# Optimization experiments

Hardware: AMD Instinct MI355X
Metric: run time of the kernel (lower is better)

Reference implementation:

```python
import jax, jax.numpy as jnp
import numpy as np

N, E = 10000, 320000
D, H, C = 256, 8, 32   # dim, heads, head_dim (dim//num_head)
DE, DF = 64, 1024      # edge_dim, dim_ff


def setup_inputs() -> dict:
    key = jax.random.key(0)
    ks = jax.random.split(key, 32)
    s = 0.05
    n = lambda k, shp: jax.random.normal(k, shp, jnp.float32) * s
    inp = {
        "nf": jax.random.normal(ks[0], (N, D), jnp.float32),
        "ei": jax.random.randint(ks[1], (2, E), 0, N),
        "ew": jax.random.normal(ks[2], (E, DE), jnp.float32),
        # GATConv 1
        "lin1": n(ks[3], (D, H * C)), "le1": n(ks[4], (DE, H * C)),
        "asrc1": n(ks[5], (H, C)), "adst1": n(ks[6], (H, C)), "aedge1": n(ks[7], (H, C)),
        "b1": jnp.zeros((H * C,), jnp.float32),
        # GATConv 2
        "lin2": n(ks[8], (D, H * C)), "le2": n(ks[9], (DE, H * C)),
        "asrc2": n(ks[10], (H, C)), "adst2": n(ks[11], (H, C)), "aedge2": n(ks[12], (H, C)),
        "b2": jnp.zeros((H * C,), jnp.float32),
        # LayerNorms
        "g1": jnp.ones((D,), jnp.float32), "be1": jnp.zeros((D,), jnp.float32),
        "g2": jnp.ones((D,), jnp.float32), "be2": jnp.zeros((D,), jnp.float32),
        "g3": jnp.ones((D,), jnp.float32), "be3": jnp.zeros((D,), jnp.float32),
        # FFN
        "w1": n(ks[13], (D, DF)), "fb1": jnp.zeros((DF,), jnp.float32),
        "w2": n(ks[14], (DF, D)), "fb2": jnp.zeros((D,), jnp.float32),
    }
    return inp


def _ln(x, g, b, eps=1e-6):
    # annotated-transformer LayerNorm: unbiased std, eps added to std
    mu = x.mean(-1, keepdims=True)
    sd = jnp.std(x, axis=-1, ddof=1, keepdims=True)
    return g * (x - mu) / (sd + eps) + b


def _gat(x, src, dst, ea, W, We, a_s, a_d, a_e, bias):
    # PyG GATConv with edge_dim, add_self_loops=True, fill_value='mean', concat=True
    ones = jnp.ones((src.shape[0], 1), x.dtype)
    cnt = jax.ops.segment_sum(ones, dst, num_segments=N)
    loop_attr = jax.ops.segment_sum(ea, dst, num_segments=N) / jnp.maximum(cnt, 1.0)
    idx = jnp.arange(N)
    srcf = jnp.concatenate([src, idx])
    dstf = jnp.concatenate([dst, idx])
    eaf = jnp.concatenate([ea, loop_attr], axis=0)          # [E+N, DE]
    xs = (x @ W).reshape(N, H, C)                            # [N,H,C]
    ef = (eaf @ We).reshape(-1, H, C)                        # [E+N,H,C]
    a_src = (xs * a_s).sum(-1)                               # [N,H]
    a_dst = (xs * a_d).sum(-1)                               # [N,H]
    alpha = a_src[srcf] + a_dst[dstf] + (ef * a_e).sum(-1)   # [E+N,H]
    alpha = jax.nn.leaky_relu(alpha, 0.2)
    m = jax.ops.segment_max(alpha, dstf, num_segments=N)     # segment softmax
    ex = jnp.exp(alpha - m[dstf])
    den = jax.ops.segment_sum(ex, dstf, num_segments=N)
    w = ex / (den[dstf] + 1e-16)                             # [E+N,H]
    out = jax.ops.segment_sum(w[:, :, None] * xs[srcf], dstf, num_segments=N)
    return out.reshape(N, H * C) + bias


def reference(nf, ei, ew, lin1, le1, asrc1, adst1, aedge1, b1,
              lin2, le2, asrc2, adst2, aedge2, b2,
              g1, be1, g2, be2, g3, be3, w1, fb1, w2, fb2):
    src, dst = ei[0], ei[1]
    h = _gat(nf, src, dst, ew, lin1, le1, asrc1, adst1, aedge1, b1)
    nf = nf + jax.nn.leaky_relu(_ln(h, g1, be1), 0.01)
    h = _gat(nf, src, dst, ew, lin2, le2, asrc2, adst2, aedge2, b2)
    nf = nf + jax.nn.leaky_relu(_ln(h, g2, be2), 0.01)
    h = jax.nn.relu(nf @ w1 + fb1) @ w2 + fb2
    nf = nf + jax.nn.leaky_relu(_ln(h, g3, be3), 0.01)
    return nf
```

## Files before the change

### kernel.cpp

```cpp
#include <hip/hip_runtime.h>
#include <hip/hip_bf16.h>
#include <math.h>

#define D 256
#define H 8
#define C 32
#define DE 64
#define DF 1024

static inline size_t align_up(size_t x, size_t a) { return (x + a - 1) / a * a; }

typedef __attribute__((ext_vector_type(8))) short short8;
typedef __attribute__((ext_vector_type(4))) float f32x4;

__device__ inline unsigned short f2b(float x) {
    __hip_bfloat16 h = __float2bfloat16(x);
    return *reinterpret_cast<unsigned short*>(&h);
}
__device__ inline float b2f(unsigned short u) {
    return __uint_as_float(((unsigned int)u) << 16);
}

__global__ void deg_kernel(const int* __restrict__ dst, int* __restrict__ deg, int E) {
    int e = blockIdx.x * 256 + threadIdx.x;
    if (e < E) atomicAdd(&deg[dst[e]], 1);
}

__global__ void partial_sum_kernel(const int* __restrict__ deg, int* __restrict__ part, int n) {
    int i = blockIdx.x * 256 + threadIdx.x;
    int v = (i < n) ? deg[i] : 0;
    for (int o = 1; o < 64; o <<= 1) v += __shfl_xor(v, o);
    __shared__ int w4[4];
    if ((threadIdx.x & 63) == 0) w4[threadIdx.x >> 6] = v;
    __syncthreads();
    if (threadIdx.x == 0) part[blockIdx.x] = w4[0] + w4[1] + w4[2] + w4[3];
}

__global__ void scan_part_kernel(int* __restrict__ part, int nb) {
    __shared__ int buf[256];
    int t = threadIdx.x;
    buf[t] = (t < nb) ? part[t] : 0;
    __syncthreads();
    for (int s = 1; s < 256; s <<= 1) {
        int v = (t >= s) ? buf[t - s] : 0;
        __syncthreads();
        buf[t] += v;
        __syncthreads();
    }
    int excl = (t == 0) ? 0 : buf[t - 1];
    if (t < nb) part[t] = excl;
}

__global__ void scan_final_kernel(const int* __restrict__ deg, const int* __restrict__ part,
                                  int* __restrict__ off, int* __restrict__ cursor, int n) {
    int b = blockIdx.x, t = threadIdx.x, i = b * 256 + t;
    __shared__ int buf[256];
    int v = (i < n) ? deg[i] : 0;
    buf[t] = v;
    __syncthreads();
    for (int s = 1; s < 256; s <<= 1) {
        int x = (t >= s) ? buf[t - s] : 0;
        __syncthreads();
        buf[t] += x;
        __syncthreads();
    }
    int excl = part[b] + buf[t] - v;
    if (i < n) { off[i] = excl; cursor[i] = excl; }
    if (i == n - 1) off[n] = excl + v;
}

__global__ void fill_kernel(const int* __restrict__ src, const int* __restrict__ dst,
                            int* __restrict__ cursor, int* __restrict__ eid,
                            int* __restrict__ src_csr, int E) {
    int e = blockIdx.x * 256 + threadIdx.x;
    if (e < E) {
        int p = atomicAdd(&cursor[dst[e]], 1);
        eid[p] = e;
        src_csr[p] = src[e];
    }
}

__global__ void prep_kernel(const float* __restrict__ lin1, const float* __restrict__ lin2,
                            const float* __restrict__ w1, const float* __restrict__ w2,
                            const float* __restrict__ le1, const float* __restrict__ ae1,
                            const float* __restrict__ le2, const float* __restrict__ ae2,
                            const float* __restrict__ nf0,
                            unsigned short* __restrict__ lin1T, unsigned short* __restrict__ lin2T,
                            unsigned short* __restrict__ w1T, unsigned short* __restrict__ w2T,
                            unsigned short* __restrict__ MeT, unsigned short* __restrict__ Abf,
                            size_t n_valid, size_t n_total) {
    int b = blockIdx.x;
    if (b > 640) {
        size_t i = ((size_t)(b - 641) * 256 + threadIdx.x) * 8;
        if (i >= n_total) return;
        ushort4 o0, o1;
        if (i < n_valid) {
            float4 a = *(const float4*)&nf0[i];
            float4 bb = *(const float4*)&nf0[i + 4];
            o0.x = f2b(a.x); o0.y = f2b(a.y); o0.z = f2b(a.z); o0.w = f2b(a.w);
            o1.x = f2b(bb.x); o1.y = f2b(bb.y); o1.z = f2b(bb.z); o1.w = f2b(bb.w);
        } else {
            o0.x = o0.y = o0.z = o0.w = 0;
            o1 = o0;
        }
        *(ushort4*)&Abf[i] = o0;
        *(ushort4*)&Abf[i + 4] = o1;
        return;
    }
    if (b == 640) {
        for (int t = threadIdx.x; t < 512; t += 256) {
            int d = t >> 3, h = t & 7;
            float s1 = 0.f, s2 = 0.f;
            for (int c = 0; c < C; ++c) {
                s1 += le1[d * (H * C) + h * C + c] * ae1[h * C + c];
                s2 += le2[d * (H * C) + h * C + c] * ae2[h * C + c];
            }
            MeT[h * 64 + d] = f2b(s1);
            MeT[(8 + h) * 64 + d] = f2b(s2);
        }
        return;
    }
    __shared__ float tile[32][33];
    const float* in; unsigned short* outp; int K, N, tt;
    if (b < 64)       { in = lin1; outp = lin1T; K = D;  N = D;  tt = b; }
    else if (b < 128) { in = lin2; outp = lin2T; K = D;  N = D;  tt = b - 64; }
    else if (b < 384) { in = w1;   outp = w1T;   K = D;  N = DF; tt = b - 128; }
    else              { in = w2;   outp = w2T;   K = DF; N = D;  tt = b - 384; }
    int ntn = N >> 5;
    int bn = (tt % ntn) * 32, bk = (tt / ntn) * 32;
    int tx = threadIdx.x & 31, ty = threadIdx.x >> 5;
    for (int i = ty; i < 32; i += 8)
        tile[i][tx] = in[(size_t)(bk + i) * N + bn + tx];
    __syncthreads();
    for (int i = ty; i < 32; i += 8)
        outp[(size_t)(bn + i) * K + bk + tx] = f2b(tile[tx][i]);
}

template<int BM>
__global__ __launch_bounds__(256) void mfma_gemm_kernel(
    const unsigned short* __restrict__ A, const unsigned short* __restrict__ BT,
    const float* __restrict__ bias, float* __restrict__ Cf, unsigned short* __restrict__ Cb,
    int M, int Nc, int K, int relu,
    const float* __restrict__ a_s, const float* __restrict__ a_d,
    float* __restrict__ asrcO, float* __restrict__ adstO) {
    constexpr int NR = (BM == 128) ? 4 : 2;
    constexpr int AI = BM / 32;
    __shared__ unsigned short As[BM * 64];
    __shared__ unsigned short Bs[128 * 64];
    int t = threadIdx.x;
    int lane = t & 63, w = t >> 6;
    int gm0 = blockIdx.x * BM, gn0 = blockIdx.y * 128;
    f32x4 acc[4][NR] = {};
    int srow = lane >> 3, scol = (lane & 7) * 8;
    int wm = (BM == 128) ? (w >> 1) * 64 : 0;
    int wn = (BM == 128) ? (w & 1) * 64 : w * 32;
    int fr = lane & 15, fk = (lane >> 4) * 8;

    for (int k0 = 0; k0 < K; k0 += 64) {
        __syncthreads();
#pragma unroll
        for (int i = 0; i < AI; ++i) {
            int rb = w * (8 * AI) + i * 8;
            const unsigned short* ga = A + (size_t)(gm0 + rb + srow) * K + k0 + scol;
            __builtin_amdgcn_global_load_lds(
                (const __attribute__((address_space(1))) unsigned int*)ga,
                (__attribute__((address_space(3))) unsigned int*)&As[rb * 64], 16, 0, 0);
        }
#pragma unroll
        for (int i = 0; i < 4; ++i) {
            int rb = w * 32 + i * 8;
            const unsigned short* gb = BT + (size_t)(gn0 + rb + srow) * K + k0 + scol;
            __builtin_amdgcn_global_load_lds(
                (const __attribute__((address_space(1))) unsigned int*)gb,
                (__attribute__((address_space(3))) unsigned int*)&Bs[rb * 64], 16, 0, 0);
        }
        __syncthreads();
#pragma unroll
        for (int kk = 0; kk < 64; kk += 32) {
            short8 a[4], b[NR];
#pragma unroll
            for (int m = 0; m < 4; ++m)
                a[m] = *(const short8*)&As[(wm + m * 16 + fr) * 64 + kk + fk];
#pragma unroll
            for (int n = 0; n < NR; ++n)
                b[n] = *(const short8*)&Bs[(wn + n * 16 + fr) * 64 + kk + fk];
#pragma unroll
            for (int m = 0; m < 4; ++m)
#pragma unroll
                for (int n = 0; n < NR; ++n)
                    acc[m][n] = __builtin_amdgcn_mfma_f32_16x16x32_bf16(a[m], b[n], acc[m][n], 0, 0, 0);
        }
    }
    int fcol = lane & 15, frow4 = (lane >> 4) * 4;
#pragma unroll
    for (int m = 0; m < 4; ++m) {
#pragma unroll
        for (int i = 0; i < 4; ++i) {
            int gr = gm0 + wm + m * 16 + frow4 + i;
            if (gr >= M) continue;
#pragma unroll
            for (int n = 0; n < NR; ++n) {
                int gc = gn0 + wn + n * 16 + fcol;
                float v = acc[m][n][i];
                if (bias) v += bias[gc];
                if (relu) v = fmaxf(v, 0.f);
                if (Cb) Cb[(size_t)gr * Nc + gc] = f2b(v);
                else    Cf[(size_t)gr * Nc + gc] = v;
            }
        }
    }
    if (BM == 64 && a_s) {
        int head = (gn0 >> 5) + w;
        float as0 = a_s[head * 32 + fcol], as1 = a_s[head * 32 + 16 + fcol];
        float ad0 = a_d[head * 32 + fcol], ad1 = a_d[head * 32 + 16 + fcol];
#pragma unroll
        for (int m = 0; m < 4; ++m) {
#pragma unroll
            for (int i = 0; i < 4; ++i) {
                float vs = acc[m][0][i] * as0 + acc[m][1][i] * as1;
                float vd = acc[m][0][i] * ad0 + acc[m][1][i] * ad1;
#pragma unroll
                for (int o = 1; o < 16; o <<= 1) {
                    vs += __shfl_xor(vs, o);
                    vd += __shfl_xor(vd, o);
                }
                int r = gm0 + m * 16 + frow4 + i;
                if (fcol == 0 && r < M) {
                    asrcO[r * 8 + head] = vs;
                    adstO[r * 8 + head] = vd;
                }
            }
        }
    }
}

__global__ __launch_bounds__(256) void ffn2_ln_kernel(
    const unsigned short* __restrict__ A, const unsigned short* __restrict__ BT,
    const float* __restrict__ bias, const float* __restrict__ nf_in,
    const float* __restrict__ gamma, const float* __restrict__ beta,
    float* __restrict__ out, int M) {
    __shared__ unsigned short As[64 * 64];
    __shared__ unsigned short Bs[256 * 64];
    __shared__ float redS1[4][64], redS2[4][64];
    __shared__ float muS[64], invS[64];
    int t = threadIdx.x, lane = t & 63, w = t >> 6;
    int gm0 = blockIdx.x * 64;
    f32x4 acc[4][4] = {};
    int srow = lane >> 3, scol = (lane & 7) * 8;
    int wn = w * 64;
    int fr = lane & 15, fk = (lane >> 4) * 8;
    for (int k0 = 0; k0 < DF; k0 += 64) {
        __syncthreads();
#pragma unroll
        for (int i = 0; i < 2; ++i) {
            int rb = w * 16 + i * 8;
            const unsigned short* ga = A + (size_t)(gm0 + rb + srow) * DF + k0 + scol;
            __builtin_amdgcn_global_load_lds(
                (const __attribute__((address_space(1))) unsigned int*)ga,
                (__attribute__((address_space(3))) unsigned int*)&As[rb * 64], 16, 0, 0);
        }
#pragma unroll
        for (int i = 0; i < 8; ++i) {
            int rb = w * 64 + i * 8;
            const unsigned short* gb = BT + (size_t)(rb + srow) * DF + k0 + scol;
            __builtin_amdgcn_global_load_lds(
                (const __attribute__((address_space(1))) unsigned int*)gb,
                (__attribute__((address_space(3))) unsigned int*)&Bs[rb * 64], 16, 0, 0);
        }
        __syncthreads();
#pragma unroll
        for (int kk = 0; kk < 64; kk += 32) {
            short8 a[4], b[4];
#pragma unroll
            for (int m = 0; m < 4; ++m)
                a[m] = *(const short8*)&As[(m * 16 + fr) * 64 + kk + fk];
#pragma unroll
            for (int n = 0; n < 4; ++n)
                b[n] = *(const short8*)&Bs[(wn + n * 16 + fr) * 64 + kk + fk];
#pragma unroll
            for (int m = 0; m < 4; ++m)
#pragma unroll
                for (int n = 0; n < 4; ++n)
                    acc[m][n] = __builtin_amdgcn_mfma_f32_16x16x32_bf16(a[m], b[n], acc[m][n], 0, 0, 0);
        }
    }
    int fcol = lane & 15, frow4 = (lane >> 4) * 4;
#pragma unroll
    for (int m = 0; m < 4; ++m) {
#pragma unroll
        for (int i = 0; i < 4; ++i) {
            float vs1 = 0.f, vs2 = 0.f;
#pragma unroll
            for (int n = 0; n < 4; ++n) {
                float vv = acc[m][n][i] + bias[wn + n * 16 + fcol];
                acc[m][n][i] = vv;
                vs1 += vv; vs2 += vv * vv;
            }
#pragma unroll
            for (int o = 1; o < 16; o <<= 1) {
                vs1 += __shfl_xor(vs1, o);
                vs2 += __shfl_xor(vs2, o);
            }
            if (fcol == 0) {
                redS1[w][m * 16 + frow4 + i] = vs1;
                redS2[w][m * 16 + frow4 + i] = vs2;
            }
        }
    }
    __syncthreads();
    if (t < 64) {
        float s1 = redS1[0][t] + redS1[1][t] + redS1[2][t] + redS1[3][t];
        float s2 = redS2[0][t] + redS2[1][t] + redS2[2][t] + redS2[3][t];
        float mu = s1 / 256.f;
        float var = fmaxf((s2 - 256.f * mu * mu) / 255.f, 0.f);
        muS[t] = mu;
        invS[t] = 1.f / (sqrtf(var) + 1e-6f);
    }
    __syncthreads();
#pragma unroll
    for (int m = 0; m < 4; ++m) {
#pragma unroll
        for (int i = 0; i < 4; ++i) {
            int r = m * 16 + frow4 + i;
            int gr = gm0 + r;
            if (gr >= M) continue;
            float mu = muS[r], inv = invS[r];
#pragma unroll
            for (int n = 0; n < 4; ++n) {
                int gc = wn + n * 16 + fcol;
                float y = gamma[gc] * (acc[m][n][i] - mu) * inv + beta[gc];
                y = y > 0.f ? y : 0.01f * y;
                out[(size_t)gr * D + gc] = nf_in[(size_t)gr * D + gc] + y;
            }
        }
    }
}

__global__ __launch_bounds__(256) void ealpha_mfma_kernel(const float* __restrict__ ew,
                                                          const unsigned short* __restrict__ MeT,
                                                          float* __restrict__ eAe, int E) {
    int t = threadIdx.x;
    int lane = t & 63, w = t >> 6;
    int e0 = blockIdx.x * 64 + w * 16;
    int r = lane & 15, g = lane >> 4;
    int er = e0 + r; if (er > E - 1) er = E - 1;
    const float* rowp = ew + (size_t)er * DE;
    float4 x0 = *(const float4*)&rowp[g * 8];
    float4 x1 = *(const float4*)&rowp[g * 8 + 4];
    float4 y0 = *(const float4*)&rowp[32 + g * 8];
    float4 y1 = *(const float4*)&rowp[32 + g * 8 + 4];
    short8 a0, a1;
    a0[0] = (short)f2b(x0.x); a0[1] = (short)f2b(x0.y); a0[2] = (short)f2b(x0.z); a0[3] = (short)f2b(x0.w);
    a0[4] = (short)f2b(x1.x); a0[5] = (short)f2b(x1.y); a0[6] = (short)f2b(x1.z); a0[7] = (short)f2b(x1.w);
    a1[0] = (short)f2b(y0.x); a1[1] = (short)f2b(y0.y); a1[2] = (short)f2b(y0.z); a1[3] = (short)f2b(y0.w);
    a1[4] = (short)f2b(y1.x); a1[5] = (short)f2b(y1.y); a1[6] = (short)f2b(y1.z); a1[7] = (short)f2b(y1.w);
    short8 b0 = *(const short8*)&MeT[r * 64 + g * 8];
    short8 b1 = *(const short8*)&MeT[r * 64 + 32 + g * 8];
    f32x4 acc = {};
    acc = __builtin_amdgcn_mfma_f32_16x16x32_bf16(a0, b0, acc, 0, 0, 0);
    acc = __builtin_amdgcn_mfma_f32_16x16x32_bf16(a1, b1, acc, 0, 0, 0);
#pragma unroll
    for (int i = 0; i < 4; ++i) {
        int ee = e0 + g * 4 + i;
        if (ee < E) eAe[(size_t)ee * 16 + r] = acc[i];
    }
}

__global__ void permute_ea_kernel(const float* __restrict__ eAe, const int* __restrict__ eid,
                                  float* __restrict__ eA1c, float* __restrict__ eA2c, int E) {
    int p = blockIdx.x * 256 + threadIdx.x;
    if (p >= E) return;
    int e = eid[p];
    const float4* src = (const float4*)&eAe[(size_t)e * 16];
    float4 v0 = src[0], v1 = src[1], v2 = src[2], v3 = src[3];
    float4* d1 = (float4*)&eA1c[(size_t)p * 8];
    float4* d2 = (float4*)&eA2c[(size_t)p * 8];
    d1[0] = v0; d1[1] = v1;
    d2[0] = v2; d2[1] = v3;
}

__global__ __launch_bounds__(256) void gat_node_kernel(
    const int* __restrict__ off, const int* __restrict__ src_csr,
    const float* __restrict__ eAc,
    const float* __restrict__ asrc, const float* __restrict__ adst,
    const unsigned short* __restrict__ xsb, const float* __restrict__ nf_in,
    const float* __restrict__ bias, const float* __restrict__ gamma,
    const float* __restrict__ beta, float* __restrict__ nf_out,
    unsigned short* __restrict__ nf_out_b, int N) {
    int lane = threadIdx.x & 63;
    int n = blockIdx.x * 4 + (threadIdx.x >> 6);
    if (n >= N) return;
    int e0 = off[n], e1 = off[n + 1], deg = e1 - e0;
    int h = lane & 7;
    int hw = lane >> 3;

    float adstn = adst[n * 8 + h];
    float asn = asrc[n * 8 + h];

    float acc0 = 0.f, acc1 = 0.f, acc2 = 0.f, acc3 = 0.f;
    float den0 = 0.f, easum = 0.f;
    int nb8 = (deg + 7) >> 3;

    bool act = hw < deg;
    int sp = e0 + hw;
    int s_cur = act ? src_csr[sp] : n;
    float ea_cur = act ? eAc[(size_t)sp * 8 + h] : 0.f;
    float as_cur = act ? asrc[s_cur * 8 + h] : 0.f;

    for (int it = 0; it < nb8; ++it) {
        int base = it * 8;
        bool actn = (base + 8 + hw) < deg;
        int spn = e0 + base + 8 + hw;
        int s_nx = actn ? src_csr[spn] : n;
        float ea_nx = actn ? eAc[(size_t)spn * 8 + h] : 0.f;
        float as_nx = actn ? asrc[s_nx * 8 + h] : 0.f;

        float al = as_cur + adstn + ea_cur;
        al = al > 0.f ? al : 0.2f * al;
        float ex = act ? expf(al) : 0.f;
        den0 += ex;
        easum += ea_cur;

        int lim = deg - base; if (lim > 8) lim = 8;
        if (lim == 8) {
#pragma unroll
            for (int kk = 0; kk < 8; ++kk) {
                int sl = kk * 8 + hw;
                float exk = __shfl(ex, sl);
                int sk = __shfl(s_cur, sl);
                ushort4 u = *(const ushort4*)&xsb[(size_t)sk * D + lane * 4];
                acc0 = fmaf(exk, b2f(u.x), acc0);
                acc1 = fmaf(exk, b2f(u.y), acc1);
                acc2 = fmaf(exk, b2f(u.z), acc2);
                acc3 = fmaf(exk, b2f(u.w), acc3);
            }
        } else {
            for (int kk = 0; kk < lim; ++kk) {
                int sl = kk * 8 + hw;
                float exk = __shfl(ex, sl);
                int sk = __shfl(s_cur, sl);
                ushort4 u = *(const ushort4*)&xsb[(size_t)sk * D + lane * 4];
                acc0 = fmaf(exk, b2f(u.x), acc0);
                acc1 = fmaf(exk, b2f(u.y), acc1);
                acc2 = fmaf(exk, b2f(u.z), acc2);
                acc3 = fmaf(exk, b2f(u.w), acc3);
            }
        }
        s_cur = s_nx; ea_cur = ea_nx; as_cur = as_nx; act = actn;
    }
    den0  += __shfl_xor(den0, 8);
    den0  += __shfl_xor(den0, 16);
    den0  += __shfl_xor(den0, 32);
    easum += __shfl_xor(easum, 8);
    easum += __shfl_xor(easum, 16);
    easum += __shfl_xor(easum, 32);
    float sa = easum / (float)(deg > 0 ? deg : 1);
    float als = asn + adstn + sa;
    als = als > 0.f ? als : 0.2f * als;
    float exSelf = expf(als);
    {
        float exs = __shfl(exSelf, hw);
        ushort4 u = *(const ushort4*)&xsb[(size_t)n * D + lane * 4];
        acc0 = fmaf(exs, b2f(u.x), acc0);
        acc1 = fmaf(exs, b2f(u.y), acc1);
        acc2 = fmaf(exs, b2f(u.z), acc2);
        acc3 = fmaf(exs, b2f(u.w), acc3);
    }
    den0 += exSelf;
    float denOwn = __shfl(den0, hw);
    float inv = 1.f / (denOwn + 1e-16f);

    int t0 = lane * 4;
    float4 bi = *(const float4*)&bias[t0];
    float o0 = acc0 * inv + bi.x;
    float o1 = acc1 * inv + bi.y;
    float o2 = acc2 * inv + bi.z;
    float o3 = acc3 * inv + bi.w;

    float s1 = o0 + o1 + o2 + o3;
    float s2 = o0 * o0 + o1 * o1 + o2 * o2 + o3 * o3;
    for (int o = 1; o < 64; o <<= 1) { s1 += __shfl_xor(s1, o); s2 += __shfl_xor(s2, o); }
    float mu = s1 / 256.f;
    float var = fmaxf((s2 - 256.f * mu * mu) / 255.f, 0.f);
    float sdv = sqrtf(var) + 1e-6f;
    float4 ga = *(const float4*)&gamma[t0];
    float4 be = *(const float4*)&beta[t0];
    float4 nin = *(const float4*)&nf_in[(size_t)n * D + t0];
    float y0 = ga.x * (o0 - mu) / sdv + be.x; y0 = y0 > 0.f ? y0 : 0.01f * y0;
    float y1 = ga.y * (o1 - mu) / sdv + be.y; y1 = y1 > 0.f ? y1 : 0.01f * y1;
    float y2 = ga.z * (o2 - mu) / sdv + be.z; y2 = y2 > 0.f ? y2 : 0.01f * y2;
    float y3 = ga.w * (o3 - mu) / sdv + be.w; y3 = y3 > 0.f ? y3 : 0.01f * y3;
    float r0 = nin.x + y0, r1 = nin.y + y1, r2 = nin.z + y2, r3 = nin.w + y3;
    float4 outv; outv.x = r0; outv.y = r1; outv.z = r2; outv.w = r3;
    *(float4*)&nf_out[(size_t)n * D + t0] = outv;
    ushort4 ob; ob.x = f2b(r0); ob.y = f2b(r1); ob.z = f2b(r2); ob.w = f2b(r3);
    *(ushort4*)&nf_out_b[(size_t)n * D + t0] = ob;
}

extern "C" void kernel_launch(void* const* d_in, const int* in_sizes, int n_in,
                              void* d_out, int out_size, void* d_ws, size_t ws_size,
                              hipStream_t stream) {
    const float* nf0    = (const float*)d_in[0];
    const int*   ei     = (const int*)d_in[1];
    const float* ew     = (const float*)d_in[2];
    const float* lin1   = (const float*)d_in[3];
    const float* le1    = (const float*)d_in[4];
    const float* asrc1w = (const float*)d_in[5];
    const float* adst1w = (const float*)d_in[6];
    const float* aedge1 = (const float*)d_in[7];
    const float* b1     = (const float*)d_in[8];
    const float* lin2   = (const float*)d_in[9];
    const float* le2    = (const float*)d_in[10];
    const float* asrc2w = (const float*)d_in[11];
    const float* adst2w = (const float*)d_in[12];
    const float* aedge2 = (const float*)d_in[13];
    const float* b2     = (const float*)d_in[14];
    const float* g1     = (const float*)d_in[15];
    const float* be1    = (const float*)d_in[16];
    const float* g2     = (const float*)d_in[17];
    const float* be2    = (const float*)d_in[18];
    const float* g3     = (const float*)d_in[19];
    const float* be3    = (const float*)d_in[20];
    const float* w1     = (const float*)d_in[21];
    const float* fb1    = (const float*)d_in[22];
    const float* w2     = (const float*)d_in[23];
    const float* fb2    = (const float*)d_in[24];

    const int N = in_sizes[0] / D;
    const int E = in_sizes[1] / 2;
    const int Mpad = ((N + 127) / 128) * 128;
    const int* srcI = ei;
    const int* dstI = ei + E;

    char* ws = (char*)d_ws;
    size_t ob = 0;
    auto alloc = [&](size_t bytes) { void* p = ws + ob; ob = align_up(ob + bytes, 256); return p; };
    int*   deg     = (int*)alloc((size_t)N * 4);
    int*   csr_off = (int*)alloc((size_t)(N + 1) * 4);
    int*   cursor  = (int*)alloc((size_t)N * 4);
    int*   part    = (int*)alloc(1024);
    int*   eid     = (int*)alloc((size_t)E * 4);
    int*   src_csr = (int*)alloc((size_t)E * 4);
    unsigned short* MeT = (unsigned short*)alloc(16 * 64 * 2);
    float* asrcB   = (float*)alloc((size_t)N * H * 4);
    float* adstB   = (float*)alloc((size_t)N * H * 4);
    float* eAe     = (float*)alloc((size_t)E * 16 * 4);
    float* eA1c    = (float*)alloc((size_t)E * H * 4);
    float* eA2c    = (float*)alloc((size_t)E * H * 4);
    float* nfw     = (float*)alloc((size_t)N * D * 4);
    unsigned short* xs_b  = (unsigned short*)alloc((size_t)Mpad * D * 2);
    unsigned short* Abf   = (unsigned short*)alloc((size_t)Mpad * D * 2);
    unsigned short* lin1T = (unsigned short*)alloc((size_t)D * D * 2);
    unsigned short* lin2T = (unsigned short*)alloc((size_t)D * D * 2);
    unsigned short* w1T   = (unsigned short*)alloc((size_t)DF * D * 2);
    unsigned short* w2T   = (unsigned short*)alloc((size_t)D * DF * 2);
    unsigned short* hidden = (unsigned short*)ws;
    (void)ws_size;
    float* out = (float*)d_out;

    hipMemsetAsync(deg, 0, (size_t)N * 4, stream);

    int eb = (E + 255) / 256;
    int nb = (N + 255) / 256;
    deg_kernel<<<eb, 256, 0, stream>>>(dstI, deg, E);
    partial_sum_kernel<<<nb, 256, 0, stream>>>(deg, part, N);
    scan_part_kernel<<<1, 256, 0, stream>>>(part, nb);
    scan_final_kernel<<<nb, 256, 0, stream>>>(deg, part, csr_off, cursor, N);
    fill_kernel<<<eb, 256, 0, stream>>>(srcI, dstI, cursor, eid, src_csr, E);

    const size_t nvalid = (size_t)N * D, ntot = (size_t)Mpad * D;
    int cb = (int)((ntot / 8 + 255) / 256);
    prep_kernel<<<641 + cb, 256, 0, stream>>>(lin1, lin2, w1, w2, le1, aedge1, le2, aedge2, nf0,
                                              lin1T, lin2T, w1T, w2T, MeT, Abf, nvalid, ntot);
    ealpha_mfma_kernel<<<(E + 63) / 64, 256, 0, stream>>>(ew, MeT, eAe, E);
    permute_ea_kernel<<<eb, 256, 0, stream>>>(eAe, eid, eA1c, eA2c, E);

    int gatb = (N + 3) / 4;

    mfma_gemm_kernel<64><<<dim3(Mpad / 64, 2), 256, 0, stream>>>(
        Abf, lin1T, nullptr, nullptr, xs_b, N, D, D, 0, asrc1w, adst1w, asrcB, adstB);
    gat_node_kernel<<<gatb, 256, 0, stream>>>(csr_off, src_csr, eA1c, asrcB, adstB,
                                              xs_b, nf0, b1, g1, be1, nfw, Abf, N);
    mfma_gemm_kernel<64><<<dim3(Mpad / 64, 2), 256, 0, stream>>>(
        Abf, lin2T, nullptr, nullptr, xs_b, N, D, D, 0, asrc2w, adst2w, asrcB, adstB);
    gat_node_kernel<<<gatb, 256, 0, stream>>>(csr_off, src_csr, eA2c, asrcB, adstB,
                                              xs_b, nfw, b2, g2, be2, nfw, Abf, N);
    mfma_gemm_kernel<128><<<dim3(Mpad / 128, 8), 256, 0, stream>>>(
        Abf, w1T, fb1, nullptr, hidden, Mpad, DF, D, 1, nullptr, nullptr, nullptr, nullptr);
    ffn2_ln_kernel<<<(N + 63) / 64, 256, 0, stream>>>(hidden, w2T, fb2, nfw, g3, be3, out, N);
}
```

Before: 253.6 us.

## Fuse edge-attention permutation into MFMA kernel and batch gathers in GAT node loop

The edge-attention MFMA kernel now reads edge rows through the CSR permutation (eid) and writes the per-layer eA1c/eA2c arrays directly, so the separate permute kernel and the intermediate eAe buffer go away. This removes one launch and a full write-then-read of an E×16 float array, in exchange for gathered (non-contiguous) reads of ew rows. The GAT node loop is also restructured so that, for full 8-edge groups, all eight xsb row gathers are issued before the softmax math and next-iteration prefetch, which exposes more memory-level parallelism. This uses more registers per thread, which may reduce occupancy.

```diff
diff --git a/kernel.cpp b/kernel.cpp
--- a/kernel.cpp
+++ b/kernel.cpp
@@ -336,14 +336,16 @@
     }
 }
 
-__global__ __launch_bounds__(256) void ealpha_mfma_kernel(const float* __restrict__ ew,
-                                                          const unsigned short* __restrict__ MeT,
-                                                          float* __restrict__ eAe, int E) {
+__global__ __launch_bounds__(256) void ealpha_mfma_kernel(
+    const float* __restrict__ ew, const int* __restrict__ eid,
+    const unsigned short* __restrict__ MeT,
+    float* __restrict__ eA1c, float* __restrict__ eA2c, int E) {
     int t = threadIdx.x;
     int lane = t & 63, w = t >> 6;
-    int e0 = blockIdx.x * 64 + w * 16;
+    int p0 = blockIdx.x * 64 + w * 16;
     int r = lane & 15, g = lane >> 4;
-    int er = e0 + r; if (er > E - 1) er = E - 1;
+    int pr = p0 + r; if (pr > E - 1) pr = E - 1;
+    int er = eid[pr];
     const float* rowp = ew + (size_t)er * DE;
     float4 x0 = *(const float4*)&rowp[g * 8];
     float4 x1 = *(const float4*)&rowp[g * 8 + 4];
@@ -361,22 +363,12 @@
     acc = __builtin_amdgcn_mfma_f32_16x16x32_bf16(a1, b1, acc, 0, 0, 0);
 #pragma unroll
     for (int i = 0; i < 4; ++i) {
-        int ee = e0 + g * 4 + i;
-        if (ee < E) eAe[(size_t)ee * 16 + r] = acc[i];
-    }
-}
-
-__global__ void permute_ea_kernel(const float* __restrict__ eAe, const int* __restrict__ eid,
-                                  float* __restrict__ eA1c, float* __restrict__ eA2c, int E) {
-    int p = blockIdx.x * 256 + threadIdx.x;
-    if (p >= E) return;
-    int e = eid[p];
-    const float4* src = (const float4*)&eAe[(size_t)e * 16];
-    float4 v0 = src[0], v1 = src[1], v2 = src[2], v3 = src[3];
-    float4* d1 = (float4*)&eA1c[(size_t)p * 8];
-    float4* d2 = (float4*)&eA2c[(size_t)p * 8];
-    d1[0] = v0; d1[1] = v1;
-    d2[0] = v2; d2[1] = v3;
+        int p = p0 + g * 4 + i;
+        if (p < E) {
+            if (r < 8) eA1c[(size_t)p * 8 + r] = acc[i];
+            else       eA2c[(size_t)p * 8 + (r - 8)] = acc[i];
+        }
+    }
 }
 
 __global__ __launch_bounds__(256) void gat_node_kernel(
@@ -409,44 +401,55 @@
 
     for (int it = 0; it < nb8; ++it) {
         int base = it * 8;
-        bool actn = (base + 8 + hw) < deg;
-        int spn = e0 + base + 8 + hw;
-        int s_nx = actn ? src_csr[spn] : n;
-        float ea_nx = actn ? eAc[(size_t)spn * 8 + h] : 0.f;
-        float as_nx = actn ? asrc[s_nx * 8 + h] : 0.f;
-
-        float al = as_cur + adstn + ea_cur;
-        al = al > 0.f ? al : 0.2f * al;
-        float ex = act ? expf(al) : 0.f;
-        den0 += ex;
-        easum += ea_cur;
-
         int lim = deg - base; if (lim > 8) lim = 8;
+
         if (lim == 8) {
+            int sk[8];
+#pragma unroll
+            for (int kk = 0; kk < 8; ++kk) sk[kk] = __shfl(s_cur, kk * 8 + hw);
+            ushort4 u[8];
+#pragma unroll
+            for (int kk = 0; kk < 8; ++kk)
+                u[kk] = *(const ushort4*)&xsb[(size_t)sk[kk] * D + lane * 4];
+            bool actn = (base + 8 + hw) < deg;
+            int spn = e0 + base + 8 + hw;
+            int s_nx = actn ? src_csr[spn] : n;
+            float ea_nx = actn ? eAc[(size_t)spn * 8 + h] : 0.f;
+            float as_nx = actn ? asrc[s_nx * 8 + h] : 0.f;
+            float al = as_cur + adstn + ea_cur;
+            al = al > 0.f ? al : 0.2f * al;
+            float ex = act ? expf(al) : 0.f;
+            den0 += ex;
+            easum += ea_cur;
+            float exk[8];
+#pragma unroll
+            for (int kk = 0; kk < 8; ++kk) exk[kk] = __shfl(ex, kk * 8 + hw);
 #pragma unroll
             for (int kk = 0; kk < 8; ++kk) {
+                acc0 = fmaf(exk[kk], b2f(u[kk].x), acc0);
+                acc1 = fmaf(exk[kk], b2f(u[kk].y), acc1);
+                acc2 = fmaf(exk[kk], b2f(u[kk].z), acc2);
+                acc3 = fmaf(exk[kk], b2f(u[kk].w), acc3);
+            }
+            s_cur = s_nx; ea_cur = ea_nx; as_cur = as_nx; act = actn;
+        } else {
+            float al = as_cur + adstn + ea_cur;
+            al = al > 0.f ? al : 0.2f * al;
+            float ex = act ? expf(al) : 0.f;
+            den0 += ex;
+            easum += ea_cur;
+            for (int kk = 0; kk < lim; ++kk) {
                 int sl = kk * 8 + hw;
                 float exk = __shfl(ex, sl);
-                int sk = __shfl(s_cur, sl);
-                ushort4 u = *(const ushort4*)&xsb[(size_t)sk * D + lane * 4];
+                int skk = __shfl(s_cur, sl);
+                ushort4 u = *(const ushort4*)&xsb[(size_t)skk * D + lane * 4];
                 acc0 = fmaf(exk, b2f(u.x), acc0);
                 acc1 = fmaf(exk, b2f(u.y), acc1);
                 acc2 = fmaf(exk, b2f(u.z), acc2);
                 acc3 = fmaf(exk, b2f(u.w), acc3);
             }
-        } else {
-            for (int kk = 0; kk < lim; ++kk) {
-                int sl = kk * 8 + hw;
-                float exk = __shfl(ex, sl);
-                int sk = __shfl(s_cur, sl);
-                ushort4 u = *(const ushort4*)&xsb[(size_t)sk * D + lane * 4];
-                acc0 = fmaf(exk, b2f(u.x), acc0);
-                acc1 = fmaf(exk, b2f(u.y), acc1);
-                acc2 = fmaf(exk, b2f(u.z), acc2);
-                acc3 = fmaf(exk, b2f(u.w), acc3);
-            }
-        }
-        s_cur = s_nx; ea_cur = ea_nx; as_cur = as_nx; act = actn;
+            act = false;
+        }
     }
     den0  += __shfl_xor(den0, 8);
     den0  += __shfl_xor(den0, 16);
@@ -544,7 +547,6 @@
     unsigned short* MeT = (unsigned short*)alloc(16 * 64 * 2);
     float* asrcB   = (float*)alloc((size_t)N * H * 4);
     float* adstB   = (float*)alloc((size_t)N * H * 4);
-    float* eAe     = (float*)alloc((size_t)E * 16 * 4);
     float* eA1c    = (float*)alloc((size_t)E * H * 4);
     float* eA2c    = (float*)alloc((size_t)E * H * 4);
     float* nfw     = (float*)alloc((size_t)N * D * 4);
@@ -572,8 +574,7 @@
     int cb = (int)((ntot / 8 + 255) / 256);
     prep_kernel<<<641 + cb, 256, 0, stream>>>(lin1, lin2, w1, w2, le1, aedge1, le2, aedge2, nf0,
                                               lin1T, lin2T, w1T, w2T, MeT, Abf, nvalid, ntot);
-    ealpha_mfma_kernel<<<(E + 63) / 64, 256, 0, stream>>>(ew, MeT, eAe, E);
-    permute_ea_kernel<<<eb, 256, 0, stream>>>(eAe, eid, eA1c, eA2c, E);
+    ealpha_mfma_kernel<<<(E + 63) / 64, 256, 0, stream>>>(ew, eid, MeT, eA1c, eA2c, E);
 
     int gatb = (N + 3) / 4;
 
```

New measurement: 239.0 us. 1.06x faster.
